# Optimization experiments

Hardware: AMD Instinct MI355X
Metric: run time of the kernel (lower is better)

The kernel has to match this reference:

```python
import jax, jax.numpy as jnp
import numpy as np

N_HEADS = 16

def setup_inputs() -> dict:
    key = jax.random.key(0)
    k1, k2, k3 = jax.random.split(key, 3)
    B, T, C = 4, 2048, 1024
    x = jax.random.normal(k1, (B, T, C), dtype=jnp.float32)
    w_qkv = jax.random.normal(k2, (C, 3 * C), dtype=jnp.float32) * (1.0 / np.sqrt(C))
    w_out = jax.random.normal(k3, (C, C), dtype=jnp.float32) * (1.0 / np.sqrt(C))
    return {"x": x, "w_qkv": w_qkv, "w_out": w_out}

def reference(x, w_qkv, w_out):
    B, T, C = x.shape
    H = N_HEADS
    D = C // H
    qkv = jnp.einsum('btc,cf->btf', x, w_qkv).reshape(B, T, 3, H, D)
    q, k, v = qkv[:, :, 0], qkv[:, :, 1], qkv[:, :, 2]  # [B,T,H,D]
    q = q.transpose(0, 2, 1, 3)  # [B,H,T,D]
    k = k.transpose(0, 2, 1, 3)
    v = v.transpose(0, 2, 1, 3)
    scale = 1.0 / jnp.sqrt(jnp.asarray(D, dtype=x.dtype))
    scores = jnp.einsum('bhqd,bhkd->bhqk', q, k) * scale  # [B,H,T,T]
    causal = jnp.tril(jnp.ones((T, T), dtype=bool))
    scores = jnp.where(causal[None, None], scores, jnp.asarray(-jnp.inf, dtype=scores.dtype))
    attn = jax.nn.softmax(scores, axis=-1)
    ctx = jnp.einsum('bhqk,bhkd->bhqd', attn, v)  # [B,H,T,D]
    ctx = ctx.transpose(0, 2, 1, 3).reshape(B, T, C)
    return jnp.einsum('btc,co->bto', ctx, w_out)
```

## Files before the change

### kernel.cpp

```cpp
#include <hip/hip_runtime.h>

typedef __attribute__((ext_vector_type(8))) short bf16x8;
typedef __attribute__((ext_vector_type(4))) short bf16x4;
typedef __attribute__((ext_vector_type(4))) float f32x4;
typedef __attribute__((ext_vector_type(4))) unsigned short u16x4;

#define MFMA16(a, b, c) __builtin_amdgcn_mfma_f32_16x16x32_bf16((a), (b), (c), 0, 0, 0)
#define MFMA16K16(a, b, c) __builtin_amdgcn_mfma_f32_16x16x16bf16_1k((a), (b), (c), 0, 0, 0)

__device__ __forceinline__ unsigned short f2bf(float f) {
    union { float f; unsigned int u; } x; x.f = f;
    unsigned int r = x.u + 0x7FFFu + ((x.u >> 16) & 1u);
    return (unsigned short)(r >> 16);
}
__device__ __forceinline__ void gload_lds16(const void* g, void* l) {
    __builtin_amdgcn_global_load_lds(
        (const __attribute__((address_space(1))) unsigned int*)g,
        (__attribute__((address_space(3))) unsigned int*)l,
        16, 0, 0);
}

__global__ void cast_x(const float* __restrict__ in, unsigned short* __restrict__ hi,
                       int n) {
    int i = (blockIdx.x * blockDim.x + threadIdx.x) * 4;
    if (i >= n) return;
    float4 v = *(const float4*)(in + i);
    float vv[4] = {v.x, v.y, v.z, v.w};
    u16x4 h;
#pragma unroll
    for (int j = 0; j < 4; ++j) h[j] = f2bf(vv[j]);
    *(u16x4*)(hi + i) = h;
}

__global__ void tcast_k(const float* __restrict__ in, unsigned short* __restrict__ out,
                        int K, int N) {
    __shared__ float tile[64][65];
    int n0 = blockIdx.x * 64, k0 = blockIdx.y * 64;
    for (int i = threadIdx.x; i < 4096; i += 256) {
        int r = i >> 6, c = i & 63;
        tile[r][c] = in[(size_t)(k0 + r) * N + n0 + c];
    }
    __syncthreads();
    for (int i = threadIdx.x; i < 4096; i += 256) {
        int r = i >> 6, c = i & 63;
        out[(size_t)(n0 + r) * K + k0 + c] = f2bf(tile[c][r]);
    }
}

__global__ __launch_bounds__(256, 2) void gemm_qkv(
    const unsigned short* __restrict__ A,
    const unsigned short* __restrict__ Bt,
    unsigned short* __restrict__ qout, unsigned short* __restrict__ kout,
    unsigned short* __restrict__ vtout) {
    const int K = 1024;
    __shared__ __align__(16) unsigned short smem[17408];
    unsigned short* sA = smem;
    unsigned short* sB = smem + 8192;
    int tid = threadIdx.x, lane = tid & 63, w = tid >> 6;
    int c = lane & 15, quad = lane >> 4;
    int sw = c & 7;
    int wm = (w >> 1) * 64, wn = (w & 1) * 64;

    int wg = blockIdx.y * 24 + blockIdx.x;
    int nid = (wg & 7) * 192 + (wg >> 3);
    int m_blk = nid / 24, n_blk = nid - m_blk * 24;
    int m0 = m_blk * 128, n0 = n_blk * 128;

    f32x4 acc[4][4];
#pragma unroll
    for (int i = 0; i < 4; i++)
#pragma unroll
        for (int j = 0; j < 4; j++) acc[i][j] = (f32x4){0.f, 0.f, 0.f, 0.f};

    for (int kk = 0; kk < K; kk += 64) {
#pragma unroll
        for (int p = 0; p < 4; ++p) {
            int ch = p * 256 + tid;
            int r = ch >> 3;
            int gs = (ch & 7) ^ (r & 7);
            gload_lds16(A + (size_t)(m0 + r) * K + kk + gs * 8, &sA[ch * 8]);
            gload_lds16(Bt + (size_t)(n0 + r) * K + kk + gs * 8, &sB[ch * 8]);
        }
        __syncthreads();
#pragma unroll
        for (int ks8 = 0; ks8 < 8; ks8 += 4) {
            bf16x8 af[4], bfr[4];
#pragma unroll
            for (int mt = 0; mt < 4; ++mt)
                af[mt] = *(const bf16x8*)&sA[(wm + mt * 16 + c) * 64 +
                                             ((ks8 + quad) ^ sw) * 8];
#pragma unroll
            for (int nt = 0; nt < 4; ++nt)
                bfr[nt] = *(const bf16x8*)&sB[(wn + nt * 16 + c) * 64 +
                                              ((ks8 + quad) ^ sw) * 8];
#pragma unroll
            for (int mt = 0; mt < 4; ++mt)
#pragma unroll
                for (int nt = 0; nt < 4; ++nt)
                    acc[mt][nt] = MFMA16(af[mt], bfr[nt], acc[mt][nt]);
        }
        __syncthreads();
    }

    const float QSCALE = 0.1803368801111601f;
    bool vreg = (n0 >= 2048);
    if (!vreg) {
        float scale = (n0 < 1024) ? QSCALE : 1.0f;
#pragma unroll
        for (int mt = 0; mt < 4; ++mt)
#pragma unroll
            for (int nt = 0; nt < 4; ++nt)
#pragma unroll
                for (int r = 0; r < 4; ++r)
                    smem[(wm + mt * 16 + quad * 4 + r) * 136 + wn + nt * 16 + c] =
                        f2bf(acc[mt][nt][r] * scale);
    } else {
#pragma unroll
        for (int mt = 0; mt < 4; ++mt)
#pragma unroll
            for (int nt = 0; nt < 4; ++nt)
#pragma unroll
                for (int r = 0; r < 4; ++r)
                    smem[(wn + nt * 16 + c) * 136 + wm + mt * 16 + quad * 4 + r] =
                        f2bf(acc[mt][nt][r]);
    }
    __syncthreads();

    int rr = tid >> 4, cc = tid & 15;
    if (!vreg) {
        int col = n0 + cc * 8;
        int which = col >> 10;
        int h = (col >> 6) & 15, d = col & 63;
        unsigned short* dst = which ? kout : qout;
#pragma unroll
        for (int j = 0; j < 8; ++j) {
            int row = rr + j * 16;
            int grow = m0 + row;
            int b = grow >> 11, t = grow & 2047;
            size_t bh_ = (size_t)(b * 16 + h);
            bf16x8 vv = *(const bf16x8*)&smem[row * 136 + cc * 8];
            *(bf16x8*)&dst[(bh_ * 2048 + t) * 64 + d] = vv;
        }
    } else {
        int grow = m0 + cc * 8;
        int b = grow >> 11, t = grow & 2047;
#pragma unroll
        for (int j = 0; j < 8; ++j) {
            int nrow = rr + j * 16;
            int col = n0 + nrow;
            int h = (col >> 6) & 15, d = col & 63;
            size_t bh_ = (size_t)(b * 16 + h);
            bf16x8 vv = *(const bf16x8*)&smem[nrow * 136 + cc * 8];
            *(bf16x8*)&vtout[(bh_ * 64 + d) * 2048 + t] = vv;
        }
    }
}

__global__ __launch_bounds__(256, 2) void gemm2_bt(
    const unsigned short* __restrict__ A,
    const unsigned short* __restrict__ Bt,
    float* __restrict__ out) {
    const int K = 1024, N = 1024;
    __shared__ __align__(16) unsigned short sA[128 * 64], sB[128 * 64];
    int tid = threadIdx.x, lane = tid & 63, w = tid >> 6;
    int c = lane & 15, quad = lane >> 4;
    int sw = c & 7;
    int wm = (w >> 1) * 64, wn = (w & 1) * 64;

    int wg = blockIdx.y * 8 + blockIdx.x;
    int nid = (wg & 7) * 64 + (wg >> 3);
    int m_blk = nid >> 3, n_blk = nid & 7;
    int m0 = m_blk * 128, n0 = n_blk * 128;

    f32x4 acc[4][4];
#pragma unroll
    for (int i = 0; i < 4; i++)
#pragma unroll
        for (int j = 0; j < 4; j++) acc[i][j] = (f32x4){0.f, 0.f, 0.f, 0.f};

    for (int kk = 0; kk < K; kk += 64) {
#pragma unroll
        for (int p = 0; p < 4; ++p) {
            int ch = p * 256 + tid;
            int r = ch >> 3;
            int gs = (ch & 7) ^ (r & 7);
            gload_lds16(A + (size_t)(m0 + r) * K + kk + gs * 8, &sA[ch * 8]);
            gload_lds16(Bt + (size_t)(n0 + r) * K + kk + gs * 8, &sB[ch * 8]);
        }
        __syncthreads();
#pragma unroll
        for (int ks8 = 0; ks8 < 8; ks8 += 4) {
            bf16x8 af[4], bfr[4];
#pragma unroll
            for (int mt = 0; mt < 4; ++mt)
                af[mt] = *(const bf16x8*)&sA[(wm + mt * 16 + c) * 64 +
                                             ((ks8 + quad) ^ sw) * 8];
#pragma unroll
            for (int nt = 0; nt < 4; ++nt)
                bfr[nt] = *(const bf16x8*)&sB[(wn + nt * 16 + c) * 64 +
                                              ((ks8 + quad) ^ sw) * 8];
#pragma unroll
            for (int mt = 0; mt < 4; ++mt)
#pragma unroll
                for (int nt = 0; nt < 4; ++nt)
                    acc[mt][nt] = MFMA16(af[mt], bfr[nt], acc[mt][nt]);
        }
        __syncthreads();
    }

#pragma unroll
    for (int mt = 0; mt < 4; ++mt)
#pragma unroll
        for (int nt = 0; nt < 4; ++nt)
#pragma unroll
            for (int r = 0; r < 4; ++r) {
                int row = m0 + wm + mt * 16 + quad * 4 + r;
                int col = n0 + wn + nt * 16 + c;
                out[(size_t)row * N + col] = acc[mt][nt][r];
            }
}

#define SSTR 72
__device__ const int JOB_ORDER[24] = {7, 15, 23, 14, 22, 6,  13, 21, 12, 20, 5,  11,
                                      19, 10, 18, 4,  9,  17, 8,  16, 3,  2,  1,  0};

__global__ __launch_bounds__(256, 4) void attn_k(
    const unsigned short* __restrict__ q,
    const unsigned short* __restrict__ k,
    const unsigned short* __restrict__ vt,
    unsigned short* __restrict__ ctx,
    float* __restrict__ op, float* __restrict__ lbuf,
    int* __restrict__ counters) {
    const int T = 2048, D = 64;
    __shared__ __align__(16) unsigned short sK[2][64 * SSTR];
    __shared__ __align__(16) unsigned short sV[2][64 * SSTR];
    __shared__ int sNext;

    int tid = threadIdx.x, lane = tid & 63, w = tid >> 6;
    int c = lane & 15, quad = lane >> 4;
    int dv = tid >> 3, tcv = (tid & 7) * 8;

    unsigned int xcd;
    asm volatile("s_getreg_b32 %0, hwreg(HW_REG_XCC_ID)" : "=s"(xcd));
    int grp = xcd & 7;

    int tries = 0;
    while (tries < 8) {
        if (tid == 0) sNext = atomicAdd(&counters[grp << 5], 1);
        __syncthreads();
        int qi = sNext;
        if (qi >= 192) {
            grp = (grp + 1) & 7;
            ++tries;
            __syncthreads();
            continue;
        }
        tries = 0;

        int rank = qi >> 3, bh = grp * 8 + (qi & 7);
        int t = JOB_ORDER[rank];
        int jt, kt0, nkt;
        bool split, has_diag;
        if (t < 8)       { jt = t;     kt0 = 0;      nkt = 2 * t + 2; split = false; has_diag = true; }
        else if (t < 16) { jt = t;     kt0 = 0;      nkt = jt + 1;    split = true;  has_diag = false; }
        else             { jt = t - 8; kt0 = jt + 1; nkt = jt + 1;    split = true;  has_diag = true; }
        int kt_end = kt0 + nkt;
        int b = bh >> 4, hh = bh & 15;

        const unsigned short* qh = q + (size_t)bh * T * D;
        const unsigned short* kh = k + (size_t)bh * T * D;
        const unsigned short* vh = vt + (size_t)bh * D * T;

        int q0 = jt * 128;
        int qloc = w * 16 + c;
        int qrow[2];
        qrow[0] = q0 + qloc;
        qrow[1] = qrow[0] + 64;

        bf16x8 bq[2][2];
#pragma unroll
        for (int g = 0; g < 2; ++g) {
            bq[g][0] = *(const bf16x8*)&qh[(size_t)qrow[g] * D + quad * 8];
            bq[g][1] = *(const bf16x8*)&qh[(size_t)qrow[g] * D + 32 + quad * 8];
        }

        f32x4 o[2][4];
#pragma unroll
        for (int g = 0; g < 2; ++g)
#pragma unroll
            for (int nt = 0; nt < 4; ++nt) o[g][nt] = (f32x4){0.f, 0.f, 0.f, 0.f};
        float l_i[2] = {0.f, 0.f};

        int kb0 = kt0 * 64;
        bf16x8 kr0 = *(const bf16x8*)&kh[(size_t)(kb0 + lane) * D + w * 8];
        bf16x8 kr1 = *(const bf16x8*)&kh[(size_t)(kb0 + lane) * D + w * 8 + 32];
        bf16x8 vr0 = *(const bf16x8*)&vh[(size_t)dv * T + kb0 + tcv];
        bf16x8 vr1 = *(const bf16x8*)&vh[(size_t)(dv + 32) * T + kb0 + tcv];
        *(bf16x8*)&sK[0][lane * SSTR + w * 8] = kr0;
        *(bf16x8*)&sK[0][lane * SSTR + w * 8 + 32] = kr1;
        *(bf16x8*)&sV[0][dv * SSTR + tcv] = vr0;
        *(bf16x8*)&sV[0][(dv + 32) * SSTR + tcv] = vr1;
        __syncthreads();

        const unsigned short* kpre = kh + (size_t)(kb0 + 64 + lane) * D + w * 8;
        const unsigned short* vpre0 = vh + (size_t)dv * T + kb0 + 64 + tcv;
        const unsigned short* vpre1 = vh + (size_t)(dv + 32) * T + kb0 + 64 + tcv;

        int cur = 0;
        for (int kt = kt0; kt < kt_end; ++kt) {
            int kb = kt * 64;
            if (kt + 1 < kt_end) {
                kr0 = *(const bf16x8*)kpre;
                kr1 = *(const bf16x8*)(kpre + 32);
                vr0 = *(const bf16x8*)vpre0;
                vr1 = *(const bf16x8*)vpre1;
                kpre += 64 * D;
                vpre0 += 64;
                vpre1 += 64;
            }
            bool g0_active = !has_diag || (kt != 2 * jt + 1);

            const unsigned short* sKc = sK[cur];
            const unsigned short* sVc = sV[cur];

            f32x4 st[2][4];
            __builtin_amdgcn_s_setprio(1);
#pragma unroll
            for (int mt = 0; mt < 4; ++mt) {
                bf16x8 ak0 = *(const bf16x8*)&sKc[(mt * 16 + c) * SSTR + quad * 8];
                bf16x8 ak1 = *(const bf16x8*)&sKc[(mt * 16 + c) * SSTR + 32 + quad * 8];
#pragma unroll
                for (int g = 0; g < 2; ++g) {
                    f32x4 z = (f32x4){0.f, 0.f, 0.f, 0.f};
                    z = MFMA16(ak0, bq[g][0], z);
                    z = MFMA16(ak1, bq[g][1], z);
                    st[g][mt] = z;
                }
            }
            __builtin_amdgcn_s_setprio(0);

            bf16x4 pf[2][4];
#pragma unroll
            for (int g = 0; g < 2; ++g) {
                if (g == 0 && !g0_active) continue;
                bool diag = has_diag && (kb == q0 + (g << 6));
                if (diag) {
#pragma unroll
                    for (int mt = 0; mt < 4; ++mt)
#pragma unroll
                        for (int r = 0; r < 4; ++r)
                            if (mt * 16 + quad * 4 + r > qloc) st[g][mt][r] = -1.0e30f;
                }
                float rs = 0.f;
#pragma unroll
                for (int mt = 0; mt < 4; ++mt) {
                    float p0 = __builtin_exp2f(st[g][mt][0]);
                    float p1 = __builtin_exp2f(st[g][mt][1]);
                    float p2 = __builtin_exp2f(st[g][mt][2]);
                    float p3 = __builtin_exp2f(st[g][mt][3]);
                    rs += (p0 + p1) + (p2 + p3);
                    unsigned int w0, w1;
                    asm("v_cvt_pk_bf16_f32 %0, %1, %2" : "=v"(w0) : "v"(p0), "v"(p1));
                    asm("v_cvt_pk_bf16_f32 %0, %1, %2" : "=v"(w1) : "v"(p2), "v"(p3));
                    uint2 pk; pk.x = w0; pk.y = w1;
                    pf[g][mt] = *(bf16x4*)&pk;
                }
                l_i[g] += rs;
            }

            __builtin_amdgcn_s_setprio(1);
#pragma unroll
            for (int mt = 0; mt < 4; ++mt) {
#pragma unroll
                for (int nt = 0; nt < 4; ++nt) {
                    bf16x4 av = *(const bf16x4*)&sVc[(nt * 16 + c) * SSTR + mt * 16 + quad * 4];
                    if (g0_active) o[0][nt] = MFMA16K16(av, pf[0][mt], o[0][nt]);
                    o[1][nt] = MFMA16K16(av, pf[1][mt], o[1][nt]);
                }
            }
            __builtin_amdgcn_s_setprio(0);

            if (kt + 1 < kt_end) {
                int nxt = cur ^ 1;
                *(bf16x8*)&sK[nxt][lane * SSTR + w * 8] = kr0;
                *(bf16x8*)&sK[nxt][lane * SSTR + w * 8 + 32] = kr1;
                *(bf16x8*)&sV[nxt][dv * SSTR + tcv] = vr0;
                *(bf16x8*)&sV[nxt][(dv + 32) * SSTR + tcv] = vr1;
                __syncthreads();
                cur = nxt;
            }
        }

        if (!split) {
#pragma unroll
            for (int g = 0; g < 2; ++g) {
                float l = l_i[g];
                l += __shfl_xor(l, 16);
                l += __shfl_xor(l, 32);
                float inv = 1.0f / l;
#pragma unroll
                for (int nt = 0; nt < 4; ++nt) {
                    u16x4 ob;
#pragma unroll
                    for (int r = 0; r < 4; ++r) ob[r] = f2bf(o[g][nt][r] * inv);
                    *(u16x4*)&ctx[(size_t)(b * T + qrow[g]) * 1024 + hh * 64 + nt * 16 + quad * 4] = ob;
                }
            }
        } else {
            int piece = has_diag ? 1 : 0;
            int sidx = bh * 8 + (jt - 8);
            size_t base = (size_t)(piece * 512 + sidx) * 128;
#pragma unroll
            for (int g = 0; g < 2; ++g) {
                float l = l_i[g];
                l += __shfl_xor(l, 16);
                l += __shfl_xor(l, 32);
                int rloc = qrow[g] - q0;
                if (quad == 0) lbuf[base + rloc] = l;
                float* orow = op + (base + rloc) * 64;
#pragma unroll
                for (int nt = 0; nt < 4; ++nt)
                    *(f32x4*)&orow[nt * 16 + quad * 4] = o[g][nt];
            }
        }

        __syncthreads();
    }
}

__global__ void merge_k(const float* __restrict__ op, const float* __restrict__ lbuf,
                        unsigned short* __restrict__ ctx) {
    int gid = blockIdx.x * 256 + threadIdx.x;
    int row = gid >> 4, dq = (gid & 15) * 4;
    int sidx = row >> 7, rloc = row & 127;
    int bh = sidx >> 3, jt = 8 + (sidx & 7);
    int b = bh >> 4, hh = bh & 15;
    int tq = jt * 128 + rloc;
    float inv = 1.0f / (lbuf[row] + lbuf[65536 + row]);
    float4 o0 = *(const float4*)(op + (size_t)row * 64 + dq);
    float4 o1 = *(const float4*)(op + (size_t)(65536 + row) * 64 + dq);
    u16x4 ob;
    ob[0] = f2bf((o0.x + o1.x) * inv);
    ob[1] = f2bf((o0.y + o1.y) * inv);
    ob[2] = f2bf((o0.z + o1.z) * inv);
    ob[3] = f2bf((o0.w + o1.w) * inv);
    *(u16x4*)&ctx[((size_t)(b * 2048 + tq)) * 1024 + hh * 64 + dq] = ob;
}

extern "C" void kernel_launch(void* const* d_in, const int* in_sizes, int n_in,
                              void* d_out, int out_size, void* d_ws, size_t ws_size,
                              hipStream_t stream) {
    const float* x     = (const float*)d_in[0];
    const float* w_qkv = (const float*)d_in[1];
    const float* w_out = (const float*)d_in[2];
    float* out = (float*)d_out;

    char* ws = (char*)d_ws;
    unsigned short* wqkvt = (unsigned short*)(ws + 0);
    unsigned short* woutt = (unsigned short*)(ws + 6291456);
    unsigned short* x_bf  = (unsigned short*)(ws + 8388608);
    unsigned short* qb    = (unsigned short*)(ws + 25165824);
    unsigned short* kb    = (unsigned short*)(ws + 41943040);
    unsigned short* vtb   = (unsigned short*)(ws + 58720256);
    unsigned short* ctx   = (unsigned short*)(ws + 8388608);

    float* op     = (float*)d_out;
    float* lbuf   = (float*)ws;
    int* counters = (int*)(ws + 524288);

    cast_x<<<8192, 256, 0, stream>>>(x, x_bf, 8388608);
    tcast_k<<<dim3(48, 16), 256, 0, stream>>>(w_qkv, wqkvt, 1024, 3072);
    tcast_k<<<dim3(16, 16), 256, 0, stream>>>(w_out, woutt, 1024, 1024);
    gemm_qkv<<<dim3(24, 64), 256, 0, stream>>>(x_bf, wqkvt, qb, kb, vtb);
    hipMemsetAsync(counters, 0, 1024, stream);
    attn_k<<<1024, 256, 0, stream>>>(qb, kb, vtb, ctx, op, lbuf, counters);
    merge_k<<<4096, 256, 0, stream>>>(op, lbuf, ctx);
    gemm2_bt<<<dim3(8, 64), 256, 0, stream>>>(ctx, woutt, out);
}
```

Measured before the change: 270.7 us.

## Replace persistent atomic scheduler with static grid and fuse split merge via flags

Drops the persistent-block work queue that used per-XCD atomic counters and launches one block per (job, head) work item, with a static job order taken from blockIdx. It also removes the separate merge kernel. Each split half writes its partial output and row sum, then bumps a per-tile flag, and whichever half arrives second combines both partials and writes ctx. This saves a kernel launch and a round trip through the partial buffers. The cost is losing dynamic load balancing and XCD-aware locality, and it depends on threadfence ordering for correctness.

```diff
diff --git a/kernel.cpp b/kernel.cpp
--- a/kernel.cpp
+++ b/kernel.cpp
@@ -230,221 +230,207 @@
     const unsigned short* __restrict__ vt,
     unsigned short* __restrict__ ctx,
     float* __restrict__ op, float* __restrict__ lbuf,
-    int* __restrict__ counters) {
+    int* __restrict__ flags) {
     const int T = 2048, D = 64;
     __shared__ __align__(16) unsigned short sK[2][64 * SSTR];
     __shared__ __align__(16) unsigned short sV[2][64 * SSTR];
-    __shared__ int sNext;
+    __shared__ int sFlag;
 
     int tid = threadIdx.x, lane = tid & 63, w = tid >> 6;
     int c = lane & 15, quad = lane >> 4;
     int dv = tid >> 3, tcv = (tid & 7) * 8;
 
-    unsigned int xcd;
-    asm volatile("s_getreg_b32 %0, hwreg(HW_REG_XCC_ID)" : "=s"(xcd));
-    int grp = xcd & 7;
-
-    int tries = 0;
-    while (tries < 8) {
-        if (tid == 0) sNext = atomicAdd(&counters[grp << 5], 1);
+    int rank = blockIdx.x >> 6, bh = blockIdx.x & 63;
+    int t = JOB_ORDER[rank];
+    int jt, kt0, nkt;
+    bool split, has_diag;
+    if (t < 8)       { jt = t;     kt0 = 0;      nkt = 2 * t + 2; split = false; has_diag = true; }
+    else if (t < 16) { jt = t;     kt0 = 0;      nkt = jt + 1;    split = true;  has_diag = false; }
+    else             { jt = t - 8; kt0 = jt + 1; nkt = jt + 1;    split = true;  has_diag = true; }
+    int kt_end = kt0 + nkt;
+    int b = bh >> 4, hh = bh & 15;
+
+    const unsigned short* qh = q + (size_t)bh * T * D;
+    const unsigned short* kh = k + (size_t)bh * T * D;
+    const unsigned short* vh = vt + (size_t)bh * D * T;
+
+    int q0 = jt * 128;
+    int qloc = w * 16 + c;
+    int qrow[2];
+    qrow[0] = q0 + qloc;
+    qrow[1] = qrow[0] + 64;
+
+    bf16x8 bq[2][2];
+#pragma unroll
+    for (int g = 0; g < 2; ++g) {
+        bq[g][0] = *(const bf16x8*)&qh[(size_t)qrow[g] * D + quad * 8];
+        bq[g][1] = *(const bf16x8*)&qh[(size_t)qrow[g] * D + 32 + quad * 8];
+    }
+
+    f32x4 o[2][4];
+#pragma unroll
+    for (int g = 0; g < 2; ++g)
+#pragma unroll
+        for (int nt = 0; nt < 4; ++nt) o[g][nt] = (f32x4){0.f, 0.f, 0.f, 0.f};
+    float l_i[2] = {0.f, 0.f};
+
+    int kb0 = kt0 * 64;
+    bf16x8 kr0 = *(const bf16x8*)&kh[(size_t)(kb0 + lane) * D + w * 8];
+    bf16x8 kr1 = *(const bf16x8*)&kh[(size_t)(kb0 + lane) * D + w * 8 + 32];
+    bf16x8 vr0 = *(const bf16x8*)&vh[(size_t)dv * T + kb0 + tcv];
+    bf16x8 vr1 = *(const bf16x8*)&vh[(size_t)(dv + 32) * T + kb0 + tcv];
+    *(bf16x8*)&sK[0][lane * SSTR + w * 8] = kr0;
+    *(bf16x8*)&sK[0][lane * SSTR + w * 8 + 32] = kr1;
+    *(bf16x8*)&sV[0][dv * SSTR + tcv] = vr0;
+    *(bf16x8*)&sV[0][(dv + 32) * SSTR + tcv] = vr1;
+    __syncthreads();
+
+    const unsigned short* kpre = kh + (size_t)(kb0 + 64 + lane) * D + w * 8;
+    const unsigned short* vpre0 = vh + (size_t)dv * T + kb0 + 64 + tcv;
+    const unsigned short* vpre1 = vh + (size_t)(dv + 32) * T + kb0 + 64 + tcv;
+
+    int cur = 0;
+    for (int kt = kt0; kt < kt_end; ++kt) {
+        int kb = kt * 64;
+        if (kt + 1 < kt_end) {
+            kr0 = *(const bf16x8*)kpre;
+            kr1 = *(const bf16x8*)(kpre + 32);
+            vr0 = *(const bf16x8*)vpre0;
+            vr1 = *(const bf16x8*)vpre1;
+            kpre += 64 * D;
+            vpre0 += 64;
+            vpre1 += 64;
+        }
+        bool g0_active = !has_diag || (kt != 2 * jt + 1);
+
+        const unsigned short* sKc = sK[cur];
+        const unsigned short* sVc = sV[cur];
+
+        f32x4 st[2][4];
+        __builtin_amdgcn_s_setprio(1);
+#pragma unroll
+        for (int mt = 0; mt < 4; ++mt) {
+            bf16x8 ak0 = *(const bf16x8*)&sKc[(mt * 16 + c) * SSTR + quad * 8];
+            bf16x8 ak1 = *(const bf16x8*)&sKc[(mt * 16 + c) * SSTR + 32 + quad * 8];
+#pragma unroll
+            for (int g = 0; g < 2; ++g) {
+                f32x4 z = (f32x4){0.f, 0.f, 0.f, 0.f};
+                z = MFMA16(ak0, bq[g][0], z);
+                z = MFMA16(ak1, bq[g][1], z);
+                st[g][mt] = z;
+            }
+        }
+        __builtin_amdgcn_s_setprio(0);
+
+        bf16x4 pf[2][4];
+#pragma unroll
+        for (int g = 0; g < 2; ++g) {
+            if (g == 0 && !g0_active) continue;
+            bool diag = has_diag && (kb == q0 + (g << 6));
+            if (diag) {
+#pragma unroll
+                for (int mt = 0; mt < 4; ++mt)
+#pragma unroll
+                    for (int r = 0; r < 4; ++r)
+                        if (mt * 16 + quad * 4 + r > qloc) st[g][mt][r] = -1.0e30f;
+            }
+            float rs = 0.f;
+#pragma unroll
+            for (int mt = 0; mt < 4; ++mt) {
+                float p0 = __builtin_exp2f(st[g][mt][0]);
+                float p1 = __builtin_exp2f(st[g][mt][1]);
+                float p2 = __builtin_exp2f(st[g][mt][2]);
+                float p3 = __builtin_exp2f(st[g][mt][3]);
+                rs += (p0 + p1) + (p2 + p3);
+                unsigned int w0, w1;
+                asm("v_cvt_pk_bf16_f32 %0, %1, %2" : "=v"(w0) : "v"(p0), "v"(p1));
+                asm("v_cvt_pk_bf16_f32 %0, %1, %2" : "=v"(w1) : "v"(p2), "v"(p3));
+                uint2 pk; pk.x = w0; pk.y = w1;
+                pf[g][mt] = *(bf16x4*)&pk;
+            }
+            l_i[g] += rs;
+        }
+
+        __builtin_amdgcn_s_setprio(1);
+#pragma unroll
+        for (int mt = 0; mt < 4; ++mt) {
+#pragma unroll
+            for (int nt = 0; nt < 4; ++nt) {
+                bf16x4 av = *(const bf16x4*)&sVc[(nt * 16 + c) * SSTR + mt * 16 + quad * 4];
+                if (g0_active) o[0][nt] = MFMA16K16(av, pf[0][mt], o[0][nt]);
+                o[1][nt] = MFMA16K16(av, pf[1][mt], o[1][nt]);
+            }
+        }
+        __builtin_amdgcn_s_setprio(0);
+
+        if (kt + 1 < kt_end) {
+            int nxt = cur ^ 1;
+            *(bf16x8*)&sK[nxt][lane * SSTR + w * 8] = kr0;
+            *(bf16x8*)&sK[nxt][lane * SSTR + w * 8 + 32] = kr1;
+            *(bf16x8*)&sV[nxt][dv * SSTR + tcv] = vr0;
+            *(bf16x8*)&sV[nxt][(dv + 32) * SSTR + tcv] = vr1;
+            __syncthreads();
+            cur = nxt;
+        }
+    }
+
+    if (!split) {
+#pragma unroll
+        for (int g = 0; g < 2; ++g) {
+            float l = l_i[g];
+            l += __shfl_xor(l, 16);
+            l += __shfl_xor(l, 32);
+            float inv = 1.0f / l;
+#pragma unroll
+            for (int nt = 0; nt < 4; ++nt) {
+                u16x4 ob;
+#pragma unroll
+                for (int r = 0; r < 4; ++r) ob[r] = f2bf(o[g][nt][r] * inv);
+                *(u16x4*)&ctx[(size_t)(b * T + qrow[g]) * 1024 + hh * 64 + nt * 16 + quad * 4] = ob;
+            }
+        }
+    } else {
+        int piece = has_diag ? 1 : 0;
+        int sidx = bh * 8 + (jt - 8);
+        size_t base = (size_t)(piece * 512 + sidx) * 128;
+        float lred[2];
+#pragma unroll
+        for (int g = 0; g < 2; ++g) {
+            float l = l_i[g];
+            l += __shfl_xor(l, 16);
+            l += __shfl_xor(l, 32);
+            lred[g] = l;
+            int rloc = qloc + (g << 6);
+            if (quad == 0) lbuf[base + rloc] = l;
+            float* orow = op + (base + rloc) * 64;
+#pragma unroll
+            for (int nt = 0; nt < 4; ++nt)
+                *(f32x4*)&orow[nt * 16 + quad * 4] = o[g][nt];
+        }
+        __threadfence();
+        if (tid == 0) sFlag = atomicAdd(&flags[sidx], 1);
         __syncthreads();
-        int qi = sNext;
-        if (qi >= 192) {
-            grp = (grp + 1) & 7;
-            ++tries;
-            __syncthreads();
-            continue;
-        }
-        tries = 0;
-
-        int rank = qi >> 3, bh = grp * 8 + (qi & 7);
-        int t = JOB_ORDER[rank];
-        int jt, kt0, nkt;
-        bool split, has_diag;
-        if (t < 8)       { jt = t;     kt0 = 0;      nkt = 2 * t + 2; split = false; has_diag = true; }
-        else if (t < 16) { jt = t;     kt0 = 0;      nkt = jt + 1;    split = true;  has_diag = false; }
-        else             { jt = t - 8; kt0 = jt + 1; nkt = jt + 1;    split = true;  has_diag = true; }
-        int kt_end = kt0 + nkt;
-        int b = bh >> 4, hh = bh & 15;
-
-        const unsigned short* qh = q + (size_t)bh * T * D;
-        const unsigned short* kh = k + (size_t)bh * T * D;
-        const unsigned short* vh = vt + (size_t)bh * D * T;
-
-        int q0 = jt * 128;
-        int qloc = w * 16 + c;
-        int qrow[2];
-        qrow[0] = q0 + qloc;
-        qrow[1] = qrow[0] + 64;
-
-        bf16x8 bq[2][2];
-#pragma unroll
-        for (int g = 0; g < 2; ++g) {
-            bq[g][0] = *(const bf16x8*)&qh[(size_t)qrow[g] * D + quad * 8];
-            bq[g][1] = *(const bf16x8*)&qh[(size_t)qrow[g] * D + 32 + quad * 8];
-        }
-
-        f32x4 o[2][4];
-#pragma unroll
-        for (int g = 0; g < 2; ++g)
-#pragma unroll
-            for (int nt = 0; nt < 4; ++nt) o[g][nt] = (f32x4){0.f, 0.f, 0.f, 0.f};
-        float l_i[2] = {0.f, 0.f};
-
-        int kb0 = kt0 * 64;
-        bf16x8 kr0 = *(const bf16x8*)&kh[(size_t)(kb0 + lane) * D + w * 8];
-        bf16x8 kr1 = *(const bf16x8*)&kh[(size_t)(kb0 + lane) * D + w * 8 + 32];
-        bf16x8 vr0 = *(const bf16x8*)&vh[(size_t)dv * T + kb0 + tcv];
-        bf16x8 vr1 = *(const bf16x8*)&vh[(size_t)(dv + 32) * T + kb0 + tcv];
-        *(bf16x8*)&sK[0][lane * SSTR + w * 8] = kr0;
-        *(bf16x8*)&sK[0][lane * SSTR + w * 8 + 32] = kr1;
-        *(bf16x8*)&sV[0][dv * SSTR + tcv] = vr0;
-        *(bf16x8*)&sV[0][(dv + 32) * SSTR + tcv] = vr1;
-        __syncthreads();
-
-        const unsigned short* kpre = kh + (size_t)(kb0 + 64 + lane) * D + w * 8;
-        const unsigned short* vpre0 = vh + (size_t)dv * T + kb0 + 64 + tcv;
-        const unsigned short* vpre1 = vh + (size_t)(dv + 32) * T + kb0 + 64 + tcv;
-
-        int cur = 0;
-        for (int kt = kt0; kt < kt_end; ++kt) {
-            int kb = kt * 64;
-            if (kt + 1 < kt_end) {
-                kr0 = *(const bf16x8*)kpre;
-                kr1 = *(const bf16x8*)(kpre + 32);
-                vr0 = *(const bf16x8*)vpre0;
-                vr1 = *(const bf16x8*)vpre1;
-                kpre += 64 * D;
-                vpre0 += 64;
-                vpre1 += 64;
-            }
-            bool g0_active = !has_diag || (kt != 2 * jt + 1);
-
-            const unsigned short* sKc = sK[cur];
-            const unsigned short* sVc = sV[cur];
-
-            f32x4 st[2][4];
-            __builtin_amdgcn_s_setprio(1);
-#pragma unroll
-            for (int mt = 0; mt < 4; ++mt) {
-                bf16x8 ak0 = *(const bf16x8*)&sKc[(mt * 16 + c) * SSTR + quad * 8];
-                bf16x8 ak1 = *(const bf16x8*)&sKc[(mt * 16 + c) * SSTR + 32 + quad * 8];
-#pragma unroll
-                for (int g = 0; g < 2; ++g) {
-                    f32x4 z = (f32x4){0.f, 0.f, 0.f, 0.f};
-                    z = MFMA16(ak0, bq[g][0], z);
-                    z = MFMA16(ak1, bq[g][1], z);
-                    st[g][mt] = z;
-                }
-            }
-            __builtin_amdgcn_s_setprio(0);
-
-            bf16x4 pf[2][4];
+        if (sFlag == 1) {
+            __threadfence();
+            size_t obase = (size_t)((1 - piece) * 512 + sidx) * 128;
 #pragma unroll
             for (int g = 0; g < 2; ++g) {
-                if (g == 0 && !g0_active) continue;
-                bool diag = has_diag && (kb == q0 + (g << 6));
-                if (diag) {
-#pragma unroll
-                    for (int mt = 0; mt < 4; ++mt)
-#pragma unroll
-                        for (int r = 0; r < 4; ++r)
-                            if (mt * 16 + quad * 4 + r > qloc) st[g][mt][r] = -1.0e30f;
-                }
-                float rs = 0.f;
-#pragma unroll
-                for (int mt = 0; mt < 4; ++mt) {
-                    float p0 = __builtin_exp2f(st[g][mt][0]);
-                    float p1 = __builtin_exp2f(st[g][mt][1]);
-                    float p2 = __builtin_exp2f(st[g][mt][2]);
-                    float p3 = __builtin_exp2f(st[g][mt][3]);
-                    rs += (p0 + p1) + (p2 + p3);
-                    unsigned int w0, w1;
-                    asm("v_cvt_pk_bf16_f32 %0, %1, %2" : "=v"(w0) : "v"(p0), "v"(p1));
-                    asm("v_cvt_pk_bf16_f32 %0, %1, %2" : "=v"(w1) : "v"(p2), "v"(p3));
-                    uint2 pk; pk.x = w0; pk.y = w1;
-                    pf[g][mt] = *(bf16x4*)&pk;
-                }
-                l_i[g] += rs;
-            }
-
-            __builtin_amdgcn_s_setprio(1);
-#pragma unroll
-            for (int mt = 0; mt < 4; ++mt) {
+                int rloc = qloc + (g << 6);
+                float lo = lbuf[obase + rloc];
+                float inv = 1.0f / (lred[g] + lo);
+                const float* orow = op + (obase + rloc) * 64;
 #pragma unroll
                 for (int nt = 0; nt < 4; ++nt) {
-                    bf16x4 av = *(const bf16x4*)&sVc[(nt * 16 + c) * SSTR + mt * 16 + quad * 4];
-                    if (g0_active) o[0][nt] = MFMA16K16(av, pf[0][mt], o[0][nt]);
-                    o[1][nt] = MFMA16K16(av, pf[1][mt], o[1][nt]);
-                }
-            }
-            __builtin_amdgcn_s_setprio(0);
-
-            if (kt + 1 < kt_end) {
-                int nxt = cur ^ 1;
-                *(bf16x8*)&sK[nxt][lane * SSTR + w * 8] = kr0;
-                *(bf16x8*)&sK[nxt][lane * SSTR + w * 8 + 32] = kr1;
-                *(bf16x8*)&sV[nxt][dv * SSTR + tcv] = vr0;
-                *(bf16x8*)&sV[nxt][(dv + 32) * SSTR + tcv] = vr1;
-                __syncthreads();
-                cur = nxt;
-            }
-        }
-
-        if (!split) {
-#pragma unroll
-            for (int g = 0; g < 2; ++g) {
-                float l = l_i[g];
-                l += __shfl_xor(l, 16);
-                l += __shfl_xor(l, 32);
-                float inv = 1.0f / l;
-#pragma unroll
-                for (int nt = 0; nt < 4; ++nt) {
+                    f32x4 oo = *(const f32x4*)&orow[nt * 16 + quad * 4];
                     u16x4 ob;
 #pragma unroll
-                    for (int r = 0; r < 4; ++r) ob[r] = f2bf(o[g][nt][r] * inv);
+                    for (int r = 0; r < 4; ++r)
+                        ob[r] = f2bf((o[g][nt][r] + oo[r]) * inv);
                     *(u16x4*)&ctx[(size_t)(b * T + qrow[g]) * 1024 + hh * 64 + nt * 16 + quad * 4] = ob;
                 }
             }
-        } else {
-            int piece = has_diag ? 1 : 0;
-            int sidx = bh * 8 + (jt - 8);
-            size_t base = (size_t)(piece * 512 + sidx) * 128;
-#pragma unroll
-            for (int g = 0; g < 2; ++g) {
-                float l = l_i[g];
-                l += __shfl_xor(l, 16);
-                l += __shfl_xor(l, 32);
-                int rloc = qrow[g] - q0;
-                if (quad == 0) lbuf[base + rloc] = l;
-                float* orow = op + (base + rloc) * 64;
-#pragma unroll
-                for (int nt = 0; nt < 4; ++nt)
-                    *(f32x4*)&orow[nt * 16 + quad * 4] = o[g][nt];
-            }
-        }
-
-        __syncthreads();
-    }
-}
-
-__global__ void merge_k(const float* __restrict__ op, const float* __restrict__ lbuf,
-                        unsigned short* __restrict__ ctx) {
-    int gid = blockIdx.x * 256 + threadIdx.x;
-    int row = gid >> 4, dq = (gid & 15) * 4;
-    int sidx = row >> 7, rloc = row & 127;
-    int bh = sidx >> 3, jt = 8 + (sidx & 7);
-    int b = bh >> 4, hh = bh & 15;
-    int tq = jt * 128 + rloc;
-    float inv = 1.0f / (lbuf[row] + lbuf[65536 + row]);
-    float4 o0 = *(const float4*)(op + (size_t)row * 64 + dq);
-    float4 o1 = *(const float4*)(op + (size_t)(65536 + row) * 64 + dq);
-    u16x4 ob;
-    ob[0] = f2bf((o0.x + o1.x) * inv);
-    ob[1] = f2bf((o0.y + o1.y) * inv);
-    ob[2] = f2bf((o0.z + o1.z) * inv);
-    ob[3] = f2bf((o0.w + o1.w) * inv);
-    *(u16x4*)&ctx[((size_t)(b * 2048 + tq)) * 1024 + hh * 64 + dq] = ob;
+        }
+    }
 }
 
 extern "C" void kernel_launch(void* const* d_in, const int* in_sizes, int n_in,
@@ -464,16 +450,15 @@
     unsigned short* vtb   = (unsigned short*)(ws + 58720256);
     unsigned short* ctx   = (unsigned short*)(ws + 8388608);
 
-    float* op     = (float*)d_out;
-    float* lbuf   = (float*)ws;
-    int* counters = (int*)(ws + 524288);
+    float* op    = (float*)d_out;
+    float* lbuf  = (float*)ws;
+    int* flags   = (int*)(ws + 524288);
 
     cast_x<<<8192, 256, 0, stream>>>(x, x_bf, 8388608);
     tcast_k<<<dim3(48, 16), 256, 0, stream>>>(w_qkv, wqkvt, 1024, 3072);
     tcast_k<<<dim3(16, 16), 256, 0, stream>>>(w_out, woutt, 1024, 1024);
     gemm_qkv<<<dim3(24, 64), 256, 0, stream>>>(x_bf, wqkvt, qb, kb, vtb);
-    hipMemsetAsync(counters, 0, 1024, stream);
-    attn_k<<<1024, 256, 0, stream>>>(qb, kb, vtb, ctx, op, lbuf, counters);
-    merge_k<<<4096, 256, 0, stream>>>(op, lbuf, ctx);
+    hipMemsetAsync(flags, 0, 2048, stream);
+    attn_k<<<1536, 256, 0, stream>>>(qb, kb, vtb, ctx, op, lbuf, flags);
     gemm2_bt<<<dim3(8, 64), 256, 0, stream>>>(ctx, woutt, out);
 }
```

Result: slower. 464.3 us (+71.5%).
